# Kernel tuning notes

Hardware: AMD Instinct MI355X
Metric: run time of the kernel (lower is better)

Reference implementation:

```python
import jax, jax.numpy as jnp
import numpy as np

N = 20000
M = 32          # max_neighbors
IN_DIM = 256
OUT_DIM = 256
H = 4           # num_heads
D = OUT_DIM // H  # head_dim = 64
LN_EPS = 1e-5
NEG_INF = -1.0e9


def setup_inputs() -> dict:
    key = jax.random.key(0)
    ks = jax.random.split(key, 6)
    h = jax.random.normal(ks[0], (N, IN_DIM), dtype=jnp.float32)
    neighbor_idx = jax.random.randint(ks[1], (N, M), 0, N, dtype=jnp.int32)
    neighbor_mask = jax.random.randint(ks[2], (N, M), 0, 2, dtype=jnp.int32)
    # parameters (xavier-ish scaling)
    W = jax.random.normal(ks[3], (IN_DIM, OUT_DIM), dtype=jnp.float32) / np.sqrt(IN_DIM)
    a_l = jax.random.normal(ks[4], (H, D), dtype=jnp.float32) / np.sqrt(D)
    a_r = jax.random.normal(ks[5], (H, D), dtype=jnp.float32) / np.sqrt(D)
    ln_gamma = jnp.ones((OUT_DIM,), dtype=jnp.float32)
    ln_beta = jnp.zeros((OUT_DIM,), dtype=jnp.float32)
    return {"h": h, "neighbor_idx": neighbor_idx, "neighbor_mask": neighbor_mask,
            "W": W, "a_l": a_l, "a_r": a_r, "ln_gamma": ln_gamma, "ln_beta": ln_beta}


def reference(h, neighbor_idx, neighbor_mask, W, a_l, a_r, ln_gamma, ln_beta):
    h_proj = h @ W                                   # [N, OUT_DIM]
    h_heads = h_proj.reshape(N, H, D)                # [N, H, D]
    # per-node score halves; gathering scalars instead of full features for er
    el = jnp.einsum('nhd,hd->nh', h_heads, a_l)      # [N, H]
    er_node = jnp.einsum('nhd,hd->nh', h_heads, a_r) # [N, H]
    er = er_node[neighbor_idx]                       # [N, M, H]
    e = jax.nn.leaky_relu(el[:, None, :] + er, negative_slope=0.2)  # [N, M, H]
    e = jnp.where(neighbor_mask[:, :, None] == 0, NEG_INF, e)
    alpha = jax.nn.softmax(e, axis=1)                # softmax over neighbors
    neigh_h = h_heads[neighbor_idx]                  # [N, M, H, D]
    out_heads = jnp.einsum('nmh,nmhd->nhd', alpha, neigh_h)
    H_cat = out_heads.reshape(N, OUT_DIM)
    res = h_proj                                     # in_dim == out_dim -> res_proj is None
    out = jax.nn.gelu(H_cat + res, approximate=False)
    # LayerNorm over last dim
    mu = jnp.mean(out, axis=-1, keepdims=True)
    var = jnp.var(out, axis=-1, keepdims=True)
    out = (out - mu) * jax.lax.rsqrt(var + LN_EPS) * ln_gamma + ln_beta
    return out
```

## Files before the change

### kernel.cpp

```cpp
#include <hip/hip_runtime.h>
#include <math.h>

#define N_NODES 20000
#define M_NEI   32
#define DIM     256
#define H_HEADS 4
#define D_HEAD  64
#define LN_EPS  1e-5f
#define NEG_INF -1.0e9f
#define APAD    264

using short8  = __attribute__((ext_vector_type(8))) short;
using short4v = __attribute__((ext_vector_type(4))) short;
using floatx4 = __attribute__((ext_vector_type(4))) float;
using floatx2 = __attribute__((ext_vector_type(2))) float;
using uintx4  = __attribute__((ext_vector_type(4))) unsigned int;
using intx4   = __attribute__((ext_vector_type(4))) int;

__device__ __forceinline__ float bf2f(unsigned short u) {
    union { unsigned int i; float f; } c; c.i = ((unsigned int)u) << 16; return c.f;
}
__device__ __forceinline__ float u2f(unsigned int i) {
    union { unsigned int i; float f; } c; c.i = i; return c.f;
}
__device__ __forceinline__ unsigned short f2bf(float f) {
    union { float f; unsigned int i; } c; c.f = f;
    unsigned int x = c.i;
    x += 0x7fffu + ((x >> 16) & 1u);
    return (unsigned short)(x >> 16);
}
__device__ __forceinline__ bool in_is_fp32(const void* gamma) {
    return *(const unsigned int*)gamma == 0x3F800000u;
}

__global__ void k_transpose(const void* __restrict__ W, const void* __restrict__ gamma,
                            unsigned short* __restrict__ Wt) {
    const bool f32 = in_is_fp32(gamma);
    int n = blockIdx.x;
    int k = threadIdx.x;
    float w = f32 ? ((const float*)W)[(size_t)k * DIM + n]
                  : bf2f(((const unsigned short*)W)[(size_t)k * DIM + n]);
    Wt[(size_t)n * DIM + k] = f2bf(w);
}

__global__ __launch_bounds__(256) void k_gemm(const void* __restrict__ A,
                                              const void* __restrict__ gamma,
                                              const unsigned short* __restrict__ Bt,
                                              const void* __restrict__ al,
                                              const void* __restrict__ ar,
                                              unsigned short* __restrict__ hp_h,
                                              float* __restrict__ el_h,
                                              float* __restrict__ er_h) {
    __shared__ unsigned short sA[16][APAD];
    const bool f32 = in_is_fp32(gamma);
    const int t    = threadIdx.x;
    const int m0   = blockIdx.x * 16;

    #pragma unroll
    for (int it = 0; it < 2; ++it) {
        int chunk = it * 256 + t;
        int row   = chunk >> 5;
        int c16   = chunk & 31;
        short8 v;
        if (!f32) {
            v = *(const short8*)((const unsigned short*)A + (size_t)(m0 + row) * DIM + c16 * 8);
        } else {
            const float* ap = (const float*)A + (size_t)(m0 + row) * DIM + c16 * 8;
            #pragma unroll
            for (int j = 0; j < 8; ++j) v[j] = (short)f2bf(ap[j]);
        }
        *(short8*)&sA[row][c16 * 8] = v;
    }
    __syncthreads();

    const int hd   = t >> 6;
    const int lane = t & 63;
    const int r    = lane & 15;
    const int quad = lane >> 4;
    const int n0   = hd * 64;

    floatx4 acc[4];
    #pragma unroll
    for (int c = 0; c < 4; ++c) acc[c] = (floatx4){0.f, 0.f, 0.f, 0.f};

    #pragma unroll
    for (int k0 = 0; k0 < DIM; k0 += 32) {
        short8 a = *(const short8*)&sA[r][k0 + quad * 8];
        #pragma unroll
        for (int c = 0; c < 4; ++c) {
            short8 b = *(const short8*)(Bt + (size_t)(n0 + c * 16 + r) * DIM + k0 + quad * 8);
            acc[c] = __builtin_amdgcn_mfma_f32_16x16x32_bf16(a, b, acc[c], 0, 0, 0);
        }
    }

    float alv[4], arv[4];
    #pragma unroll
    for (int c = 0; c < 4; ++c) {
        int col = n0 + c * 16 + r;
        if (f32) { alv[c] = ((const float*)al)[col]; arv[c] = ((const float*)ar)[col]; }
        else     { alv[c] = bf2f(((const unsigned short*)al)[col]);
                   arv[c] = bf2f(((const unsigned short*)ar)[col]); }
    }

    #pragma unroll
    for (int rr = 0; rr < 4; ++rr) {
        const int row = m0 + quad * 4 + rr;
        float sl = 0.f, sr = 0.f;
        #pragma unroll
        for (int c = 0; c < 4; ++c) {
            float v = acc[c][rr];
            sl += v * alv[c];
            sr += v * arv[c];
            hp_h[((size_t)hd * N_NODES + row) * D_HEAD + c * 16 + r] = f2bf(v);
        }
        #pragma unroll
        for (int off = 1; off < 16; off <<= 1) {
            sl += __shfl_xor(sl, off);
            sr += __shfl_xor(sr, off);
        }
        if (r == 0) {
            el_h[(size_t)hd * N_NODES + row] = sl;
            er_h[(size_t)hd * N_NODES + row] = sr;
        }
    }
}

__global__ __launch_bounds__(256) void k_attn_h(const int* __restrict__ nidx,
                                                const int* __restrict__ nmask,
                                                const unsigned short* __restrict__ hp_h,
                                                const float* __restrict__ el_h,
                                                const float* __restrict__ er_h,
                                                unsigned short* __restrict__ out_h) {
    __shared__ int   s_idx[32][33];
    __shared__ float s_al[32][33];

    const int hd  = blockIdx.x & 3;
    const int nb0 = (blockIdx.x >> 2) * 32;
    const int t   = threadIdx.x;

    {
        const int m   = t & 31;
        const int sub = t >> 5;
        #pragma unroll
        for (int it = 0; it < 4; ++it) {
            const int nl  = it * 8 + sub;
            const int n   = nb0 + nl;
            const int idx = nidx[(size_t)n * M_NEI + m];
            const int msk = nmask[(size_t)n * M_NEI + m];
            float e = el_h[(size_t)hd * N_NODES + n] + er_h[(size_t)hd * N_NODES + idx];
            e = (e > 0.f) ? e : 0.2f * e;
            e = msk ? e : NEG_INF;
            float mx = e;
            #pragma unroll
            for (int off = 1; off < 32; off <<= 1) mx = fmaxf(mx, __shfl_xor(mx, off, 32));
            float a = expf(e - mx);
            float sm = a;
            #pragma unroll
            for (int off = 1; off < 32; off <<= 1) sm += __shfl_xor(sm, off, 32);
            s_idx[nl][m] = idx;
            s_al[nl][m]  = a / sm;
        }
    }
    __syncthreads();

    const int wave = t >> 6;
    const int lane = t & 63;
    const int g    = lane >> 3;
    const int s    = lane & 7;
    const int nl   = wave * 8 + g;
    const int n    = nb0 + nl;
    const unsigned short* tbl = hp_h + (size_t)hd * N_NODES * D_HEAD + s * 8;

    floatx2 acc[4];
    #pragma unroll
    for (int j = 0; j < 4; ++j) acc[j] = (floatx2){0.f, 0.f};

    #pragma unroll
    for (int m = 0; m < M_NEI; ++m) {
        const int   rowi = s_idx[nl][m];
        const float aa   = s_al[nl][m];
        uintx4 u = *(const uintx4*)(tbl + (size_t)rowi * D_HEAD);
        #pragma unroll
        for (int j = 0; j < 4; ++j) {
            floatx2 f = { u2f(u[j] << 16), u2f(u[j] & 0xffff0000u) };
            acc[j] += (floatx2){aa, aa} * f;
        }
    }

    short8 o;
    #pragma unroll
    for (int j = 0; j < 4; ++j) {
        o[2 * j]     = (short)f2bf(acc[j][0]);
        o[2 * j + 1] = (short)f2bf(acc[j][1]);
    }
    *(short8*)(out_h + ((size_t)hd * N_NODES + n) * D_HEAD + s * 8) = o;
}

__global__ __launch_bounds__(256) void k_final(const unsigned short* __restrict__ hp_h,
                                               const unsigned short* __restrict__ out_h,
                                               const void* __restrict__ gamma,
                                               const void* __restrict__ beta,
                                               void* __restrict__ out) {
    const bool f32 = in_is_fp32(gamma);
    const int wave = threadIdx.x >> 6;
    const int lane = threadIdx.x & 63;
    const int n    = blockIdx.x * 4 + wave;
    const int h    = lane >> 4;
    const int d0   = (lane & 15) * 4;

    const size_t off = ((size_t)h * N_NODES + n) * D_HEAD + d0;
    short4v hv = *(const short4v*)(hp_h + off);
    short4v ov = *(const short4v*)(out_h + off);

    float x[4], s1 = 0.f, s2 = 0.f;
    #pragma unroll
    for (int i = 0; i < 4; ++i) {
        float xi = bf2f((unsigned short)ov[i]) + bf2f((unsigned short)hv[i]);
        xi = 0.5f * xi * (1.f + erff(xi * 0.70710678118654752f));
        x[i] = xi;
        s1 += xi;
        s2 += xi * xi;
    }
    #pragma unroll
    for (int offv = 1; offv < 64; offv <<= 1) {
        s1 += __shfl_xor(s1, offv);
        s2 += __shfl_xor(s2, offv);
    }
    const float mu  = s1 * (1.f / 256.f);
    float var = s2 * (1.f / 256.f) - mu * mu;
    var = fmaxf(var, 0.f);
    const float inv = rsqrtf(var + LN_EPS);

    if (f32) {
        const float* gp = (const float*)gamma + lane * 4;
        const float* bp = (const float*)beta  + lane * 4;
        float* op = (float*)out + (size_t)n * DIM + lane * 4;
        #pragma unroll
        for (int i = 0; i < 4; ++i)
            op[i] = (x[i] - mu) * inv * gp[i] + bp[i];
    } else {
        const unsigned short* gp = (const unsigned short*)gamma + lane * 4;
        const unsigned short* bp = (const unsigned short*)beta  + lane * 4;
        short4v o;
        #pragma unroll
        for (int i = 0; i < 4; ++i) {
            float y = (x[i] - mu) * inv * bf2f(gp[i]) + bf2f(bp[i]);
            o[i] = (short)f2bf(y);
        }
        *(short4v*)((unsigned short*)out + (size_t)n * DIM + lane * 4) = o;
    }
}

extern "C" void kernel_launch(void* const* d_in, const int* in_sizes, int n_in,
                              void* d_out, int out_size, void* d_ws, size_t ws_size,
                              hipStream_t stream) {
    const void* h     = d_in[0];
    const int*  nidx  = (const int*)d_in[1];
    const int*  nmask = (const int*)d_in[2];
    const void* W     = d_in[3];
    const void* al    = d_in[4];
    const void* ar    = d_in[5];
    const void* gamma = d_in[6];
    const void* beta  = d_in[7];

    unsigned short* Wt    = (unsigned short*)d_ws;
    unsigned short* hp_h  = (unsigned short*)((char*)d_ws + 131072);
    unsigned short* out_h = (unsigned short*)((char*)d_ws + 10371072);
    float* el_h = (float*)((char*)d_ws + 20611072);
    float* er_h = (float*)((char*)d_ws + 20931072);

    k_transpose<<<DIM, DIM, 0, stream>>>(W, gamma, Wt);
    k_gemm<<<N_NODES / 16, 256, 0, stream>>>(h, gamma, Wt, al, ar, hp_h, el_h, er_h);
    k_attn_h<<<H_HEADS * (N_NODES / 32), 256, 0, stream>>>(nidx, nmask, hp_h, el_h, er_h, out_h);
    k_final<<<N_NODES / 4, 256, 0, stream>>>(hp_h, out_h, gamma, beta, d_out);
}
```

Baseline: 141.4 us.

## Pack neighbor index and mask, fold residual into attention kernel

A prep kernel now also packs each neighbor index and its mask bit into one int, so the attention kernel reads one array instead of two. The attention kernel stores a byte offset and the alpha value together as an int2 in shared memory, which saves address math in the gather loop. It also adds the residual h_proj row before writing out_h, so the final kernel no longer reads hp_h. The cost is an extra pass that reads both neighbor arrays and writes a packed copy each call, plus the residual being rounded to bf16 once more before GELU.

New measurement: 140.7 us. About the same (-0.5%).

```diff
diff --git a/kernel.cpp b/kernel.cpp
--- a/kernel.cpp
+++ b/kernel.cpp
@@ -15,7 +15,6 @@
 using floatx4 = __attribute__((ext_vector_type(4))) float;
 using floatx2 = __attribute__((ext_vector_type(2))) float;
 using uintx4  = __attribute__((ext_vector_type(4))) unsigned int;
-using intx4   = __attribute__((ext_vector_type(4))) int;
 
 __device__ __forceinline__ float bf2f(unsigned short u) {
     union { unsigned int i; float f; } c; c.i = ((unsigned int)u) << 16; return c.f;
@@ -33,14 +32,22 @@
     return *(const unsigned int*)gamma == 0x3F800000u;
 }
 
-__global__ void k_transpose(const void* __restrict__ W, const void* __restrict__ gamma,
-                            unsigned short* __restrict__ Wt) {
-    const bool f32 = in_is_fp32(gamma);
-    int n = blockIdx.x;
-    int k = threadIdx.x;
-    float w = f32 ? ((const float*)W)[(size_t)k * DIM + n]
-                  : bf2f(((const unsigned short*)W)[(size_t)k * DIM + n]);
-    Wt[(size_t)n * DIM + k] = f2bf(w);
+__global__ void k_prep(const void* __restrict__ W, const void* __restrict__ gamma,
+                       const int* __restrict__ nidx, const int* __restrict__ nmask,
+                       unsigned short* __restrict__ Wt, int* __restrict__ pidx) {
+    const int b = blockIdx.x;
+    const int t = threadIdx.x;
+    if (b < DIM) {
+        const bool f32 = in_is_fp32(gamma);
+        float w = f32 ? ((const float*)W)[(size_t)t * DIM + b]
+                      : bf2f(((const unsigned short*)W)[(size_t)t * DIM + b]);
+        Wt[(size_t)b * DIM + t] = f2bf(w);
+    } else {
+        const int i = (b - DIM) * 256 + t;
+        const int idx = nidx[i];
+        const int msk = nmask[i];
+        pidx[i] = idx | (msk ? (int)0x80000000 : 0);
+    }
 }
 
 __global__ __launch_bounds__(256) void k_gemm(const void* __restrict__ A,
@@ -125,14 +132,12 @@
     }
 }
 
-__global__ __launch_bounds__(256) void k_attn_h(const int* __restrict__ nidx,
-                                                const int* __restrict__ nmask,
+__global__ __launch_bounds__(256) void k_attn_h(const int* __restrict__ pidx,
                                                 const unsigned short* __restrict__ hp_h,
                                                 const float* __restrict__ el_h,
                                                 const float* __restrict__ er_h,
                                                 unsigned short* __restrict__ out_h) {
-    __shared__ int   s_idx[32][33];
-    __shared__ float s_al[32][33];
+    __shared__ int2 s_oa[32][33];
 
     const int hd  = blockIdx.x & 3;
     const int nb0 = (blockIdx.x >> 2) * 32;
@@ -143,13 +148,13 @@
         const int sub = t >> 5;
         #pragma unroll
         for (int it = 0; it < 4; ++it) {
-            const int nl  = it * 8 + sub;
-            const int n   = nb0 + nl;
-            const int idx = nidx[(size_t)n * M_NEI + m];
-            const int msk = nmask[(size_t)n * M_NEI + m];
+            const int nl = it * 8 + sub;
+            const int n  = nb0 + nl;
+            const int v  = pidx[(size_t)n * M_NEI + m];
+            const int idx = v & 0x7fffffff;
             float e = el_h[(size_t)hd * N_NODES + n] + er_h[(size_t)hd * N_NODES + idx];
             e = (e > 0.f) ? e : 0.2f * e;
-            e = msk ? e : NEG_INF;
+            e = (v < 0) ? e : NEG_INF;
             float mx = e;
             #pragma unroll
             for (int off = 1; off < 32; off <<= 1) mx = fmaxf(mx, __shfl_xor(mx, off, 32));
@@ -157,8 +162,11 @@
             float sm = a;
             #pragma unroll
             for (int off = 1; off < 32; off <<= 1) sm += __shfl_xor(sm, off, 32);
-            s_idx[nl][m] = idx;
-            s_al[nl][m]  = a / sm;
+            int2 oa;
+            oa.x = idx * (D_HEAD * 2);
+            union { float f; int i; } c; c.f = a / sm;
+            oa.y = c.i;
+            s_oa[nl][m] = oa;
         }
     }
     __syncthreads();
@@ -169,7 +177,7 @@
     const int s    = lane & 7;
     const int nl   = wave * 8 + g;
     const int n    = nb0 + nl;
-    const unsigned short* tbl = hp_h + (size_t)hd * N_NODES * D_HEAD + s * 8;
+    const char* tbl = (const char*)hp_h + (size_t)hd * N_NODES * (D_HEAD * 2) + s * 16;
 
     floatx2 acc[4];
     #pragma unroll
@@ -177,9 +185,9 @@
 
     #pragma unroll
     for (int m = 0; m < M_NEI; ++m) {
-        const int   rowi = s_idx[nl][m];
-        const float aa   = s_al[nl][m];
-        uintx4 u = *(const uintx4*)(tbl + (size_t)rowi * D_HEAD);
+        const int2  oa = s_oa[nl][m];
+        const float aa = u2f((unsigned int)oa.y);
+        uintx4 u = *(const uintx4*)(tbl + oa.x);
         #pragma unroll
         for (int j = 0; j < 4; ++j) {
             floatx2 f = { u2f(u[j] << 16), u2f(u[j] & 0xffff0000u) };
@@ -187,6 +195,16 @@
         }
     }
 
+    {
+        uintx4 u = *(const uintx4*)((const char*)hp_h
+                     + ((size_t)hd * N_NODES + n) * (D_HEAD * 2) + s * 16);
+        #pragma unroll
+        for (int j = 0; j < 4; ++j) {
+            floatx2 f = { u2f(u[j] << 16), u2f(u[j] & 0xffff0000u) };
+            acc[j] += f;
+        }
+    }
+
     short8 o;
     #pragma unroll
     for (int j = 0; j < 4; ++j) {
@@ -196,8 +214,7 @@
     *(short8*)(out_h + ((size_t)hd * N_NODES + n) * D_HEAD + s * 8) = o;
 }
 
-__global__ __launch_bounds__(256) void k_final(const unsigned short* __restrict__ hp_h,
-                                               const unsigned short* __restrict__ out_h,
+__global__ __launch_bounds__(256) void k_final(const unsigned short* __restrict__ out_h,
                                                const void* __restrict__ gamma,
                                                const void* __restrict__ beta,
                                                void* __restrict__ out) {
@@ -209,13 +226,12 @@
     const int d0   = (lane & 15) * 4;
 
     const size_t off = ((size_t)h * N_NODES + n) * D_HEAD + d0;
-    short4v hv = *(const short4v*)(hp_h + off);
     short4v ov = *(const short4v*)(out_h + off);
 
     float x[4], s1 = 0.f, s2 = 0.f;
     #pragma unroll
     for (int i = 0; i < 4; ++i) {
-        float xi = bf2f((unsigned short)ov[i]) + bf2f((unsigned short)hv[i]);
+        float xi = bf2f((unsigned short)ov[i]);
         xi = 0.5f * xi * (1.f + erff(xi * 0.70710678118654752f));
         x[i] = xi;
         s1 += xi;
@@ -268,9 +284,10 @@
     unsigned short* out_h = (unsigned short*)((char*)d_ws + 10371072);
     float* el_h = (float*)((char*)d_ws + 20611072);
     float* er_h = (float*)((char*)d_ws + 20931072);
-
-    k_transpose<<<DIM, DIM, 0, stream>>>(W, gamma, Wt);
+    int*   pidx = (int*)((char*)d_ws + 21251072);
+
+    k_prep<<<DIM + (N_NODES * M_NEI) / 256, 256, 0, stream>>>(W, gamma, nidx, nmask, Wt, pidx);
     k_gemm<<<N_NODES / 16, 256, 0, stream>>>(h, gamma, Wt, al, ar, hp_h, el_h, er_h);
-    k_attn_h<<<H_HEADS * (N_NODES / 32), 256, 0, stream>>>(nidx, nmask, hp_h, el_h, er_h, out_h);
-    k_final<<<N_NODES / 4, 256, 0, stream>>>(hp_h, out_h, gamma, beta, d_out);
-}
+    k_attn_h<<<H_HEADS * (N_NODES / 32), 256, 0, stream>>>(pidx, hp_h, el_h, er_h, out_h);
+    k_final<<<N_NODES / 4, 256, 0, stream>>>(out_h, gamma, beta, d_out);
+}
```
